# Kernel tuning notes

Hardware: AMD Instinct MI355X
Metric: run time of the kernel (lower is better)

## Reference

```python
import jax, jax.numpy as jnp
import numpy as np

NAN_FRAC = 0.1  # fraction of entries replaced by NaN


def setup_inputs() -> dict:
    key = jax.random.key(0)
    kx, ky, kmx, kmy = jax.random.split(key, 4)
    N, M, D = 4096, 4096, 1024
    X = jax.random.normal(kx, (N, D), dtype=jnp.float32)
    Y = jax.random.normal(ky, (M, D), dtype=jnp.float32)
    X = jnp.where(jax.random.uniform(kmx, (N, D)) < NAN_FRAC, jnp.nan, X)
    Y = jnp.where(jax.random.uniform(kmy, (M, D)) < NAN_FRAC, jnp.nan, Y)
    return {"X": X, "Y": Y}


def reference(X, Y):
    # NaN-masked euclidean distances (sklearn nan_euclidean_distances), squared=False
    missing_X = jnp.isnan(X)                      # [N, D] bool
    missing_Y = jnp.isnan(Y)                      # [M, D] bool
    Xc = jnp.where(missing_X, 0.0, X)
    Yc = jnp.where(missing_Y, 0.0, Y)
    XX = Xc * Xc
    YY = Yc * Yc
    # base squared distances with zero-filled NaNs
    d = (-2.0 * (Xc @ Yc.T)
         + XX.sum(1, keepdims=True)
         + YY.sum(1, keepdims=True).T)            # [N, M]
    # remove contributions where the other side is missing
    d = d - XX @ missing_Y.astype(Xc.dtype).T
    d = d - missing_X.astype(Xc.dtype) @ YY.T
    d = jnp.clip(d, 0.0, None)
    present_X = 1.0 - missing_X.astype(Xc.dtype)  # [N, D]
    present_Y = 1.0 - missing_Y.astype(Xc.dtype)  # [M, D]
    present_count = present_X @ present_Y.T       # [N, M]
    d = jnp.where(present_count == 0, jnp.nan, d)
    pc = jnp.maximum(jnp.asarray(1.0, d.dtype), present_count)
    d = d / pc * X.shape[1]
    return jnp.sqrt(d)
```

## Files before the change

### kernel.cpp

```cpp
#include <hip/hip_runtime.h>
#include <hip/hip_bf16.h>
#include <stdint.h>


typedef __bf16 bf16_t;
typedef __attribute__((ext_vector_type(8))) __bf16 bf16x8;
typedef __attribute__((ext_vector_type(4))) float floatx4;
typedef __attribute__((ext_vector_type(16))) float floatx16;
typedef __attribute__((ext_vector_type(8))) int int32x8;

#define NROWS 4096
#define MCOLS 4096
#define DDIM  1024
#define BM 128
#define BN 128
#define BK 64

#define WS_XX ((uint32_t)0)
#define WS_XC ((uint32_t)(4  << 20))
#define WS_P  ((uint32_t)(8  << 20))
#define WS_YY ((uint32_t)(12 << 20))
#define WS_M2 ((uint32_t)(16 << 20))
#define WS_Q  ((uint32_t)(20 << 20))
#define WS_NEEDED ((size_t)(24 << 20))

#define L_XX 0
#define L_XC 8192
#define L_P  16384
#define L_YY 24576
#define L_M2 32768
#define L_Q  40960

__global__ __launch_bounds__(256)
void convert_planes_mx(const float* __restrict__ X, const float* __restrict__ Y,
                       char* __restrict__ ws) {
    int b = blockIdx.x;
    bool isX = (b < 1024);
    const float* src = isX ? X : Y;
    int rb = isX ? b : b - 1024;
    int row = rb * 4 + (threadIdx.x >> 6);
    int l = threadIdx.x & 63;
    int k0 = l << 4;

    const float4* p = (const float4*)(src + (size_t)row * DDIM + k0);
    float v[16];
    #pragma unroll
    for (int i = 0; i < 4; i++) {
        float4 t = p[i];
        v[4*i+0] = t.x; v[4*i+1] = t.y; v[4*i+2] = t.z; v[4*i+3] = t.w;
    }
    float fa[16], fb[16], fm[16];
    #pragma unroll
    for (int i = 0; i < 16; i++) {
        float x = v[i];
        bool miss = __builtin_isnan(x);
        float c = miss ? 0.f : x;
        fb[i] = c * c;
        fa[i] = isX ? c : (-2.f * c);
        fm[i] = miss ? 0.f : 1.f;
    }
    uint32_t da[4], db[4], dm[4];
    #pragma unroll
    for (int i = 0; i < 4; i++) {
        int r = __builtin_amdgcn_cvt_pk_fp8_f32(fa[4*i], fa[4*i+1], 0, 0);
        r     = __builtin_amdgcn_cvt_pk_fp8_f32(fa[4*i+2], fa[4*i+3], r, 1);
        da[i] = (uint32_t)r;
        int s = __builtin_amdgcn_cvt_pk_fp8_f32(fb[4*i], fb[4*i+1], 0, 0);
        s     = __builtin_amdgcn_cvt_pk_fp8_f32(fb[4*i+2], fb[4*i+3], s, 1);
        db[i] = (uint32_t)s;
        int m = __builtin_amdgcn_cvt_pk_fp8_f32(fm[4*i], fm[4*i+1], 0, 0);
        m     = __builtin_amdgcn_cvt_pk_fp8_f32(fm[4*i+2], fm[4*i+3], m, 1);
        dm[i] = (uint32_t)m;
    }
    uint32_t off8 = (uint32_t)row * 1024u + (uint32_t)(l >> 2) * 64u
                  + (uint32_t)((((l & 3) ^ ((row >> 1) & 3)) << 4));
    uint4 A = make_uint4(da[0], da[1], da[2], da[3]);
    uint4 B = make_uint4(db[0], db[1], db[2], db[3]);
    uint4 M = make_uint4(dm[0], dm[1], dm[2], dm[3]);
    if (isX) {
        *(uint4*)(ws + WS_XC + off8) = A;
        *(uint4*)(ws + WS_XX + off8) = B;
        *(uint4*)(ws + WS_P  + off8) = M;
    } else {
        *(uint4*)(ws + WS_M2 + off8) = A;
        *(uint4*)(ws + WS_YY + off8) = B;
        *(uint4*)(ws + WS_Q  + off8) = M;
    }
}

__device__ __forceinline__ int32x8 ld32B(const char* p0, const char* p1) {
    union { int32x8 v; int4 h[2]; } u;
    u.h[0] = *(const int4*)p0;
    u.h[1] = *(const int4*)p1;
    return u.v;
}

__global__ __launch_bounds__(256, 2)
void nan_euclid_mx(const char* __restrict__ ws, float* __restrict__ out) {
    __shared__ __align__(16) char ldsb[49152];

    const int tid = threadIdx.x, lane = tid & 63, wid = tid >> 6;
    const int l31 = lane & 31, kh = lane >> 5;
    const int wrow = (wid >> 1) * 64, wcol = (wid & 1) * 64;
    const int blockRow = blockIdx.y * BM, blockCol = blockIdx.x * BN;

    uint32_t goff[12];
    #pragma unroll
    for (int t = 0; t < 12; t++) {
        int ch = (wid * 12 + t) * 64 + lane;
        int pl = ch >> 9;
        int c2 = ch & 511;
        int row = c2 >> 2, cc = c2 & 3;
        int rg = (pl < 3 ? blockRow : blockCol) + row;
        uint32_t base = (pl == 0) ? WS_XX : (pl == 1) ? WS_XC : (pl == 2) ? WS_P
                      : (pl == 3) ? WS_YY : (pl == 4) ? WS_M2 : WS_Q;
        goff[t] = base + (uint32_t)rg * 1024u + (uint32_t)(cc << 4);
    }

    int aoff0[2], aoff1[2], boff0[2], boff1[2];
    #pragma unroll
    for (int tt = 0; tt < 2; tt++) {
        int m = wrow + tt * 32 + l31;
        int sw = (m >> 1) & 3;
        aoff0[tt] = m * 64 + (((kh * 2)     ^ sw) << 4);
        aoff1[tt] = m * 64 + (((kh * 2 + 1) ^ sw) << 4);
        int n = wcol + tt * 32 + l31;
        int swn = (n >> 1) & 3;
        boff0[tt] = n * 64 + (((kh * 2)     ^ swn) << 4);
        boff1[tt] = n * 64 + (((kh * 2 + 1) ^ swn) << 4);
    }

    floatx16 acc_d[2][2], acc_c[2][2];
    #pragma unroll
    for (int i = 0; i < 2; i++)
        #pragma unroll
        for (int j = 0; j < 2; j++)
            #pragma unroll
            for (int r = 0; r < 16; r++) { acc_d[i][j][r] = 0.f; acc_c[i][j][r] = 0.f; }

    for (int kc = 0; kc < DDIM / BK; kc++) {
        #pragma unroll
        for (int t = 0; t < 12; t++) {
            __builtin_amdgcn_global_load_lds(
                (const __attribute__((address_space(1))) void*)(ws + goff[t] + kc * 64u),
                (__attribute__((address_space(3))) void*)(ldsb + (uint32_t)((wid * 12 + t) * 1024)),
                16, 0, 0);
        }
        __syncthreads();

        int32x8 axx[2], axc[2], ap[2], byy[2], bm2[2], bq[2];
        #pragma unroll
        for (int tt = 0; tt < 2; tt++) {
            axx[tt] = ld32B(ldsb + L_XX + aoff0[tt], ldsb + L_XX + aoff1[tt]);
            axc[tt] = ld32B(ldsb + L_XC + aoff0[tt], ldsb + L_XC + aoff1[tt]);
            ap [tt] = ld32B(ldsb + L_P  + aoff0[tt], ldsb + L_P  + aoff1[tt]);
            byy[tt] = ld32B(ldsb + L_YY + boff0[tt], ldsb + L_YY + boff1[tt]);
            bm2[tt] = ld32B(ldsb + L_M2 + boff0[tt], ldsb + L_M2 + boff1[tt]);
            bq [tt] = ld32B(ldsb + L_Q  + boff0[tt], ldsb + L_Q  + boff1[tt]);
        }

        #pragma unroll
        for (int tm = 0; tm < 2; tm++)
            #pragma unroll
            for (int tn = 0; tn < 2; tn++)
                acc_d[tm][tn] = __builtin_amdgcn_mfma_scale_f32_32x32x64_f8f6f4(
                    axx[tm], bq[tn], acc_d[tm][tn], 0, 0, 0, 0x7f7f7f7f, 0, 0x7f7f7f7f);
        #pragma unroll
        for (int tm = 0; tm < 2; tm++)
            #pragma unroll
            for (int tn = 0; tn < 2; tn++)
                acc_d[tm][tn] = __builtin_amdgcn_mfma_scale_f32_32x32x64_f8f6f4(
                    ap[tm], byy[tn], acc_d[tm][tn], 0, 0, 0, 0x7f7f7f7f, 0, 0x7f7f7f7f);
        #pragma unroll
        for (int tm = 0; tm < 2; tm++)
            #pragma unroll
            for (int tn = 0; tn < 2; tn++)
                acc_d[tm][tn] = __builtin_amdgcn_mfma_scale_f32_32x32x64_f8f6f4(
                    axc[tm], bm2[tn], acc_d[tm][tn], 0, 0, 0, 0x7f7f7f7f, 0, 0x7f7f7f7f);
        #pragma unroll
        for (int tm = 0; tm < 2; tm++)
            #pragma unroll
            for (int tn = 0; tn < 2; tn++)
                acc_c[tm][tn] = __builtin_amdgcn_mfma_scale_f32_32x32x64_f8f6f4(
                    ap[tm], bq[tn], acc_c[tm][tn], 0, 0, 0, 0x7f7f7f7f, 0, 0x7f7f7f7f);

        __syncthreads();
    }

    #pragma unroll
    for (int tm = 0; tm < 2; tm++) {
        #pragma unroll
        for (int tn = 0; tn < 2; tn++) {
            int col = blockCol + wcol + tn * 32 + l31;
            #pragma unroll
            for (int r = 0; r < 16; r++) {
                int rowl = (r & 3) + 8 * (r >> 2) + 4 * kh;
                int row = blockRow + wrow + tm * 32 + rowl;
                float d = fmaxf(acc_d[tm][tn][r], 0.f);
                float c = acc_c[tm][tn][r];
                float res = (c < 0.5f) ? __builtin_nanf("")
                                       : __builtin_sqrtf(d * (float)DDIM / c);
                out[(size_t)row * MCOLS + col] = res;
            }
        }
    }
}

#define LDK 40
__global__ __launch_bounds__(256, 2)
void nan_euclid_fused(const float* __restrict__ X, const float* __restrict__ Y,
                      float* __restrict__ out) {
    typedef __attribute__((ext_vector_type(4))) __bf16 bf16x4;
    __shared__ bf16_t s_xx[BM * LDK];
    __shared__ bf16_t s_p [BM * LDK];
    __shared__ bf16_t s_xc[BM * LDK];
    __shared__ bf16_t s_q [BN * LDK];
    __shared__ bf16_t s_yy[BN * LDK];
    __shared__ bf16_t s_m2[BN * LDK];

    const int tid  = threadIdx.x;
    const int lane = tid & 63;
    const int wid  = tid >> 6;
    const int quad = lane >> 4;
    const int r16  = lane & 15;
    const int wrow = (wid >> 1) * 64;
    const int wcol = (wid & 1) * 64;
    const int blockRow = blockIdx.y * BM;
    const int blockCol = blockIdx.x * BN;

    floatx4 acc_d[4][4];
    floatx4 acc_c[4][4];
    #pragma unroll
    for (int i = 0; i < 4; i++)
        #pragma unroll
        for (int j = 0; j < 4; j++)
            #pragma unroll
            for (int r = 0; r < 4; r++) { acc_d[i][j][r] = 0.f; acc_c[i][j][r] = 0.f; }

    for (int kc = 0; kc < DDIM / 32; kc++) {
        const int kbase = kc * 32;
        #pragma unroll
        for (int i = 0; i < 4; i++) {
            int idx = tid + 256 * i;
            int row = idx >> 3;
            int c4  = idx & 7;
            const float4 v = *(const float4*)(X + (size_t)(blockRow + row) * DDIM + kbase + c4 * 4);
            bf16x4 vxc, vxx, vp;
            const float xs[4] = {v.x, v.y, v.z, v.w};
            #pragma unroll
            for (int e = 0; e < 4; e++) {
                float x = xs[e];
                bool miss = __builtin_isnan(x);
                float xc = miss ? 0.f : x;
                vxc[e] = (bf16_t)xc;
                vxx[e] = (bf16_t)(xc * xc);
                vp[e]  = miss ? (bf16_t)0.f : (bf16_t)1.f;
            }
            int off = row * LDK + c4 * 4;
            *(bf16x4*)&s_xc[off] = vxc;
            *(bf16x4*)&s_xx[off] = vxx;
            *(bf16x4*)&s_p [off] = vp;
        }
        #pragma unroll
        for (int i = 0; i < 4; i++) {
            int idx = tid + 256 * i;
            int row = idx >> 3;
            int c4  = idx & 7;
            const float4 v = *(const float4*)(Y + (size_t)(blockCol + row) * DDIM + kbase + c4 * 4);
            bf16x4 vq, vyy, vm2;
            const float ys[4] = {v.x, v.y, v.z, v.w};
            #pragma unroll
            for (int e = 0; e < 4; e++) {
                float y = ys[e];
                bool miss = __builtin_isnan(y);
                float yc = miss ? 0.f : y;
                vq[e]  = miss ? (bf16_t)0.f : (bf16_t)1.f;
                vyy[e] = (bf16_t)(yc * yc);
                vm2[e] = (bf16_t)(-2.f * yc);
            }
            int off = row * LDK + c4 * 4;
            *(bf16x4*)&s_q [off] = vq;
            *(bf16x4*)&s_yy[off] = vyy;
            *(bf16x4*)&s_m2[off] = vm2;
        }
        __syncthreads();
        bf16x8 bq[4], byy[4], bm2[4];
        #pragma unroll
        for (int tn = 0; tn < 4; tn++) {
            int off = (wcol + tn * 16 + r16) * LDK + quad * 8;
            bq[tn]  = *(const bf16x8*)&s_q [off];
            byy[tn] = *(const bf16x8*)&s_yy[off];
            bm2[tn] = *(const bf16x8*)&s_m2[off];
        }
        #pragma unroll
        for (int tm = 0; tm < 4; tm++) {
            int off = (wrow + tm * 16 + r16) * LDK + quad * 8;
            bf16x8 axx = *(const bf16x8*)&s_xx[off];
            bf16x8 ap  = *(const bf16x8*)&s_p [off];
            bf16x8 axc = *(const bf16x8*)&s_xc[off];
            #pragma unroll
            for (int tn = 0; tn < 4; tn++) {
                acc_d[tm][tn] = __builtin_amdgcn_mfma_f32_16x16x32_bf16(axx, bq[tn],  acc_d[tm][tn], 0, 0, 0);
                acc_d[tm][tn] = __builtin_amdgcn_mfma_f32_16x16x32_bf16(ap,  byy[tn], acc_d[tm][tn], 0, 0, 0);
                acc_d[tm][tn] = __builtin_amdgcn_mfma_f32_16x16x32_bf16(axc, bm2[tn], acc_d[tm][tn], 0, 0, 0);
                acc_c[tm][tn] = __builtin_amdgcn_mfma_f32_16x16x32_bf16(ap,  bq[tn],  acc_c[tm][tn], 0, 0, 0);
            }
        }
        __syncthreads();
    }
    #pragma unroll
    for (int tm = 0; tm < 4; tm++) {
        #pragma unroll
        for (int tn = 0; tn < 4; tn++) {
            int col = blockCol + wcol + tn * 16 + r16;
            #pragma unroll
            for (int r = 0; r < 4; r++) {
                int row = blockRow + wrow + tm * 16 + quad * 4 + r;
                float d = acc_d[tm][tn][r];
                float c = acc_c[tm][tn][r];
                d = fmaxf(d, 0.f);
                float res = (c < 0.5f) ? __builtin_nanf("")
                                       : __builtin_sqrtf(d * (float)DDIM / c);
                out[(size_t)row * MCOLS + col] = res;
            }
        }
    }
}

extern "C" void kernel_launch(void* const* d_in, const int* in_sizes, int n_in,
                              void* d_out, int out_size, void* d_ws, size_t ws_size,
                              hipStream_t stream) {
    const float* X = (const float*)d_in[0];
    const float* Y = (const float*)d_in[1];
    float* out = (float*)d_out;

    if (ws_size >= WS_NEEDED) {
        char* ws = (char*)d_ws;
        convert_planes_mx<<<dim3(2048), dim3(256), 0, stream>>>(X, Y, ws);
        dim3 grid(MCOLS / BN, NROWS / BM);
        nan_euclid_mx<<<grid, dim3(256), 0, stream>>>(ws, out);
    } else {
        dim3 grid(MCOLS / BN, NROWS / BM);
        nan_euclid_fused<<<grid, dim3(256), 0, stream>>>(X, Y, out);
    }
}
```

Baseline: 164.3 us.

## Double-buffer LDS tiles, swizzle block order, and reshape the fp8 conversion kernel

The main GEMM kernel now keeps two 48KB LDS buffers and issues the global-to-LDS loads for the next K chunk before running the MFMAs on the current one, cutting one barrier per step so memory latency overlaps compute. Blocks are launched on a 1D grid and remapped in strides of eight to improve L2 reuse of the X and Y planes. The conversion kernel now uses one block per row with 4-byte stores instead of 16-byte stores. The 96KB of LDS per block may stop two blocks from sharing a CU as the launch bounds request, and the narrower stores may make the conversion pass slower.

```diff
diff --git a/kernel.cpp b/kernel.cpp
--- a/kernel.cpp
+++ b/kernel.cpp
@@ -30,28 +30,22 @@
 #define L_YY 24576
 #define L_M2 32768
 #define L_Q  40960
+#define BUFSZ 49152
 
 __global__ __launch_bounds__(256)
 void convert_planes_mx(const float* __restrict__ X, const float* __restrict__ Y,
                        char* __restrict__ ws) {
     int b = blockIdx.x;
-    bool isX = (b < 1024);
+    bool isX = (b < 4096);
     const float* src = isX ? X : Y;
-    int rb = isX ? b : b - 1024;
-    int row = rb * 4 + (threadIdx.x >> 6);
-    int l = threadIdx.x & 63;
-    int k0 = l << 4;
-
-    const float4* p = (const float4*)(src + (size_t)row * DDIM + k0);
-    float v[16];
+    int row = isX ? b : b - 4096;
+    int l = threadIdx.x;
+
+    float4 t = *(const float4*)(src + (size_t)row * DDIM + l * 4);
+    float v[4] = {t.x, t.y, t.z, t.w};
+    float fa[4], fb[4], fm[4];
     #pragma unroll
     for (int i = 0; i < 4; i++) {
-        float4 t = p[i];
-        v[4*i+0] = t.x; v[4*i+1] = t.y; v[4*i+2] = t.z; v[4*i+3] = t.w;
-    }
-    float fa[16], fb[16], fm[16];
-    #pragma unroll
-    for (int i = 0; i < 16; i++) {
         float x = v[i];
         bool miss = __builtin_isnan(x);
         float c = miss ? 0.f : x;
@@ -59,32 +53,24 @@
         fa[i] = isX ? c : (-2.f * c);
         fm[i] = miss ? 0.f : 1.f;
     }
-    uint32_t da[4], db[4], dm[4];
-    #pragma unroll
-    for (int i = 0; i < 4; i++) {
-        int r = __builtin_amdgcn_cvt_pk_fp8_f32(fa[4*i], fa[4*i+1], 0, 0);
-        r     = __builtin_amdgcn_cvt_pk_fp8_f32(fa[4*i+2], fa[4*i+3], r, 1);
-        da[i] = (uint32_t)r;
-        int s = __builtin_amdgcn_cvt_pk_fp8_f32(fb[4*i], fb[4*i+1], 0, 0);
-        s     = __builtin_amdgcn_cvt_pk_fp8_f32(fb[4*i+2], fb[4*i+3], s, 1);
-        db[i] = (uint32_t)s;
-        int m = __builtin_amdgcn_cvt_pk_fp8_f32(fm[4*i], fm[4*i+1], 0, 0);
-        m     = __builtin_amdgcn_cvt_pk_fp8_f32(fm[4*i+2], fm[4*i+3], m, 1);
-        dm[i] = (uint32_t)m;
-    }
-    uint32_t off8 = (uint32_t)row * 1024u + (uint32_t)(l >> 2) * 64u
-                  + (uint32_t)((((l & 3) ^ ((row >> 1) & 3)) << 4));
-    uint4 A = make_uint4(da[0], da[1], da[2], da[3]);
-    uint4 B = make_uint4(db[0], db[1], db[2], db[3]);
-    uint4 M = make_uint4(dm[0], dm[1], dm[2], dm[3]);
+    int r = __builtin_amdgcn_cvt_pk_fp8_f32(fa[0], fa[1], 0, 0);
+    r     = __builtin_amdgcn_cvt_pk_fp8_f32(fa[2], fa[3], r, 1);
+    int s = __builtin_amdgcn_cvt_pk_fp8_f32(fb[0], fb[1], 0, 0);
+    s     = __builtin_amdgcn_cvt_pk_fp8_f32(fb[2], fb[3], s, 1);
+    int m = __builtin_amdgcn_cvt_pk_fp8_f32(fm[0], fm[1], 0, 0);
+    m     = __builtin_amdgcn_cvt_pk_fp8_f32(fm[2], fm[3], m, 1);
+
+    uint32_t sw = ((uint32_t)row >> 1) & 3u;
+    uint32_t off = (uint32_t)row * 1024u + (uint32_t)((l >> 4) << 6)
+                 + (((((uint32_t)l >> 2) & 3u) ^ sw) << 4) + (uint32_t)((l & 3) << 2);
     if (isX) {
-        *(uint4*)(ws + WS_XC + off8) = A;
-        *(uint4*)(ws + WS_XX + off8) = B;
-        *(uint4*)(ws + WS_P  + off8) = M;
+        *(uint32_t*)(ws + WS_XC + off) = (uint32_t)r;
+        *(uint32_t*)(ws + WS_XX + off) = (uint32_t)s;
+        *(uint32_t*)(ws + WS_P  + off) = (uint32_t)m;
     } else {
-        *(uint4*)(ws + WS_M2 + off8) = A;
-        *(uint4*)(ws + WS_YY + off8) = B;
-        *(uint4*)(ws + WS_Q  + off8) = M;
+        *(uint32_t*)(ws + WS_M2 + off) = (uint32_t)r;
+        *(uint32_t*)(ws + WS_YY + off) = (uint32_t)s;
+        *(uint32_t*)(ws + WS_Q  + off) = (uint32_t)m;
     }
 }
 
@@ -97,12 +83,16 @@
 
 __global__ __launch_bounds__(256, 2)
 void nan_euclid_mx(const char* __restrict__ ws, float* __restrict__ out) {
-    __shared__ __align__(16) char ldsb[49152];
+    __shared__ __align__(16) char ldsb[2 * BUFSZ];
 
     const int tid = threadIdx.x, lane = tid & 63, wid = tid >> 6;
     const int l31 = lane & 31, kh = lane >> 5;
     const int wrow = (wid >> 1) * 64, wcol = (wid & 1) * 64;
-    const int blockRow = blockIdx.y * BM, blockCol = blockIdx.x * BN;
+
+    const int bid = blockIdx.x;
+    const int swz = (bid & 7) * 128 + (bid >> 3);
+    const int blockRow = (swz >> 5) * BM;
+    const int blockCol = (swz & 31) * BN;
 
     uint32_t goff[12];
     #pragma unroll
@@ -117,17 +107,13 @@
         goff[t] = base + (uint32_t)rg * 1024u + (uint32_t)(cc << 4);
     }
 
-    int aoff0[2], aoff1[2], boff0[2], boff1[2];
+    int aoff[2], boff[2];
     #pragma unroll
     for (int tt = 0; tt < 2; tt++) {
         int m = wrow + tt * 32 + l31;
-        int sw = (m >> 1) & 3;
-        aoff0[tt] = m * 64 + (((kh * 2)     ^ sw) << 4);
-        aoff1[tt] = m * 64 + (((kh * 2 + 1) ^ sw) << 4);
+        aoff[tt] = m * 64 + ((((kh * 2)) ^ ((m >> 1) & 3)) << 4);
         int n = wcol + tt * 32 + l31;
-        int swn = (n >> 1) & 3;
-        boff0[tt] = n * 64 + (((kh * 2)     ^ swn) << 4);
-        boff1[tt] = n * 64 + (((kh * 2 + 1) ^ swn) << 4);
+        boff[tt] = n * 64 + ((((kh * 2)) ^ ((n >> 1) & 3)) << 4);
     }
 
     floatx16 acc_d[2][2], acc_c[2][2];
@@ -138,54 +124,71 @@
             #pragma unroll
             for (int r = 0; r < 16; r++) { acc_d[i][j][r] = 0.f; acc_c[i][j][r] = 0.f; }
 
-    for (int kc = 0; kc < DDIM / BK; kc++) {
-        #pragma unroll
-        for (int t = 0; t < 12; t++) {
-            __builtin_amdgcn_global_load_lds(
-                (const __attribute__((address_space(1))) void*)(ws + goff[t] + kc * 64u),
-                (__attribute__((address_space(3))) void*)(ldsb + (uint32_t)((wid * 12 + t) * 1024)),
-                16, 0, 0);
-        }
-        __syncthreads();
-
-        int32x8 axx[2], axc[2], ap[2], byy[2], bm2[2], bq[2];
-        #pragma unroll
-        for (int tt = 0; tt < 2; tt++) {
-            axx[tt] = ld32B(ldsb + L_XX + aoff0[tt], ldsb + L_XX + aoff1[tt]);
-            axc[tt] = ld32B(ldsb + L_XC + aoff0[tt], ldsb + L_XC + aoff1[tt]);
-            ap [tt] = ld32B(ldsb + L_P  + aoff0[tt], ldsb + L_P  + aoff1[tt]);
-            byy[tt] = ld32B(ldsb + L_YY + boff0[tt], ldsb + L_YY + boff1[tt]);
-            bm2[tt] = ld32B(ldsb + L_M2 + boff0[tt], ldsb + L_M2 + boff1[tt]);
-            bq [tt] = ld32B(ldsb + L_Q  + boff0[tt], ldsb + L_Q  + boff1[tt]);
-        }
-
-        #pragma unroll
-        for (int tm = 0; tm < 2; tm++)
-            #pragma unroll
-            for (int tn = 0; tn < 2; tn++)
-                acc_d[tm][tn] = __builtin_amdgcn_mfma_scale_f32_32x32x64_f8f6f4(
-                    axx[tm], bq[tn], acc_d[tm][tn], 0, 0, 0, 0x7f7f7f7f, 0, 0x7f7f7f7f);
-        #pragma unroll
-        for (int tm = 0; tm < 2; tm++)
-            #pragma unroll
-            for (int tn = 0; tn < 2; tn++)
-                acc_d[tm][tn] = __builtin_amdgcn_mfma_scale_f32_32x32x64_f8f6f4(
-                    ap[tm], byy[tn], acc_d[tm][tn], 0, 0, 0, 0x7f7f7f7f, 0, 0x7f7f7f7f);
-        #pragma unroll
-        for (int tm = 0; tm < 2; tm++)
-            #pragma unroll
-            for (int tn = 0; tn < 2; tn++)
-                acc_d[tm][tn] = __builtin_amdgcn_mfma_scale_f32_32x32x64_f8f6f4(
-                    axc[tm], bm2[tn], acc_d[tm][tn], 0, 0, 0, 0x7f7f7f7f, 0, 0x7f7f7f7f);
-        #pragma unroll
-        for (int tm = 0; tm < 2; tm++)
-            #pragma unroll
-            for (int tn = 0; tn < 2; tn++)
-                acc_c[tm][tn] = __builtin_amdgcn_mfma_scale_f32_32x32x64_f8f6f4(
-                    ap[tm], bq[tn], acc_c[tm][tn], 0, 0, 0, 0x7f7f7f7f, 0, 0x7f7f7f7f);
-
-        __syncthreads();
-    }
+    #pragma unroll
+    for (int t = 0; t < 12; t++) {
+        __builtin_amdgcn_global_load_lds(
+            (const __attribute__((address_space(1))) void*)(ws + goff[t]),
+            (__attribute__((address_space(3))) void*)(ldsb + (uint32_t)((wid * 12 + t) * 1024)),
+            16, 0, 0);
+    }
+    __syncthreads();
+
+#define KSTEP(CURB, NXTB, NKC)                                                     \
+    do {                                                                           \
+        if ((NKC) < DDIM / BK) {                                                   \
+            _Pragma("unroll")                                                      \
+            for (int t = 0; t < 12; t++) {                                         \
+                __builtin_amdgcn_global_load_lds(                                  \
+                    (const __attribute__((address_space(1))) void*)(               \
+                        ws + goff[t] + (uint32_t)(NKC) * 64u),                     \
+                    (__attribute__((address_space(3))) void*)(                     \
+                        ldsb + (NXTB) + (uint32_t)((wid * 12 + t) * 1024)),        \
+                    16, 0, 0);                                                     \
+            }                                                                      \
+        }                                                                          \
+        const char* buf = ldsb + (CURB);                                           \
+        int32x8 axx[2], axc[2], ap[2], byy[2], bm2[2], bq[2];                      \
+        _Pragma("unroll")                                                          \
+        for (int tt = 0; tt < 2; tt++) {                                           \
+            axx[tt] = ld32B(buf + L_XX + aoff[tt], buf + L_XX + (aoff[tt] ^ 16));  \
+            axc[tt] = ld32B(buf + L_XC + aoff[tt], buf + L_XC + (aoff[tt] ^ 16));  \
+            ap [tt] = ld32B(buf + L_P  + aoff[tt], buf + L_P  + (aoff[tt] ^ 16));  \
+            byy[tt] = ld32B(buf + L_YY + boff[tt], buf + L_YY + (boff[tt] ^ 16));  \
+            bm2[tt] = ld32B(buf + L_M2 + boff[tt], buf + L_M2 + (boff[tt] ^ 16));  \
+            bq [tt] = ld32B(buf + L_Q  + boff[tt], buf + L_Q  + (boff[tt] ^ 16));  \
+        }                                                                          \
+        _Pragma("unroll")                                                          \
+        for (int tm = 0; tm < 2; tm++)                                             \
+            _Pragma("unroll")                                                      \
+            for (int tn = 0; tn < 2; tn++)                                         \
+                acc_d[tm][tn] = __builtin_amdgcn_mfma_scale_f32_32x32x64_f8f6f4(   \
+                    axx[tm], bq[tn], acc_d[tm][tn], 0, 0, 0, 0x7f7f7f7f, 0, 0x7f7f7f7f); \
+        _Pragma("unroll")                                                          \
+        for (int tm = 0; tm < 2; tm++)                                             \
+            _Pragma("unroll")                                                      \
+            for (int tn = 0; tn < 2; tn++)                                         \
+                acc_d[tm][tn] = __builtin_amdgcn_mfma_scale_f32_32x32x64_f8f6f4(   \
+                    ap[tm], byy[tn], acc_d[tm][tn], 0, 0, 0, 0x7f7f7f7f, 0, 0x7f7f7f7f); \
+        _Pragma("unroll")                                                          \
+        for (int tm = 0; tm < 2; tm++)                                             \
+            _Pragma("unroll")                                                      \
+            for (int tn = 0; tn < 2; tn++)                                         \
+                acc_d[tm][tn] = __builtin_amdgcn_mfma_scale_f32_32x32x64_f8f6f4(   \
+                    axc[tm], bm2[tn], acc_d[tm][tn], 0, 0, 0, 0x7f7f7f7f, 0, 0x7f7f7f7f); \
+        _Pragma("unroll")                                                          \
+        for (int tm = 0; tm < 2; tm++)                                             \
+            _Pragma("unroll")                                                      \
+            for (int tn = 0; tn < 2; tn++)                                         \
+                acc_c[tm][tn] = __builtin_amdgcn_mfma_scale_f32_32x32x64_f8f6f4(   \
+                    ap[tm], bq[tn], acc_c[tm][tn], 0, 0, 0, 0x7f7f7f7f, 0, 0x7f7f7f7f); \
+        __syncthreads();                                                           \
+    } while (0)
+
+    for (int kc2 = 0; kc2 < DDIM / BK / 2; kc2++) {
+        KSTEP(0,     BUFSZ, 2 * kc2 + 1);
+        KSTEP(BUFSZ, 0,     2 * kc2 + 2);
+    }
+#undef KSTEP
 
     #pragma unroll
     for (int tm = 0; tm < 2; tm++) {
@@ -336,9 +339,8 @@
 
     if (ws_size >= WS_NEEDED) {
         char* ws = (char*)d_ws;
-        convert_planes_mx<<<dim3(2048), dim3(256), 0, stream>>>(X, Y, ws);
-        dim3 grid(MCOLS / BN, NROWS / BM);
-        nan_euclid_mx<<<grid, dim3(256), 0, stream>>>(ws, out);
+        convert_planes_mx<<<dim3(8192), dim3(256), 0, stream>>>(X, Y, ws);
+        nan_euclid_mx<<<dim3(1024), dim3(256), 0, stream>>>(ws, out);
     } else {
         dim3 grid(MCOLS / BN, NROWS / BM);
         nan_euclid_fused<<<grid, dim3(256), 0, stream>>>(X, Y, out);
```

Result: slower. 218.4 us (+32.9%).

## Interleave fp8 planes per row and give each convert block one row

Applied to the files above, without the earlier changes.

The workspace layout changes from six separate plane arrays to a per-row interleaved layout in which each row holds its xx, xc and mask planes contiguously (3 KB per row) for X and Y. The convert kernel now uses one block per row with 4 elements per thread and 4-byte stores, launched over 8192 blocks. The main kernel's global offsets follow the new layout, the LDS second-half offset is computed with an XOR, and MFMA sections are wrapped in s_setprio. The aim is better locality for the per-tile global-to-LDS loads and better balance in the conversion pass, at the cost of smaller 4-byte stores in the convert kernel.

```diff
diff --git a/kernel.cpp b/kernel.cpp
--- a/kernel.cpp
+++ b/kernel.cpp
@@ -16,12 +16,7 @@
 #define BN 128
 #define BK 64
 
-#define WS_XX ((uint32_t)0)
-#define WS_XC ((uint32_t)(4  << 20))
-#define WS_P  ((uint32_t)(8  << 20))
-#define WS_YY ((uint32_t)(12 << 20))
-#define WS_M2 ((uint32_t)(16 << 20))
-#define WS_Q  ((uint32_t)(20 << 20))
+#define WS_YBASE ((uint32_t)(12 << 20))
 #define WS_NEEDED ((size_t)(24 << 20))
 
 #define L_XX 0
@@ -35,23 +30,16 @@
 void convert_planes_mx(const float* __restrict__ X, const float* __restrict__ Y,
                        char* __restrict__ ws) {
     int b = blockIdx.x;
-    bool isX = (b < 1024);
+    bool isX = (b < 4096);
     const float* src = isX ? X : Y;
-    int rb = isX ? b : b - 1024;
-    int row = rb * 4 + (threadIdx.x >> 6);
-    int l = threadIdx.x & 63;
-    int k0 = l << 4;
-
-    const float4* p = (const float4*)(src + (size_t)row * DDIM + k0);
-    float v[16];
+    int row = isX ? b : b - 4096;
+    int l = threadIdx.x;
+
+    float4 t = *(const float4*)(src + (size_t)row * DDIM + l * 4);
+    float v[4] = {t.x, t.y, t.z, t.w};
+    float fa[4], fb[4], fm[4];
     #pragma unroll
     for (int i = 0; i < 4; i++) {
-        float4 t = p[i];
-        v[4*i+0] = t.x; v[4*i+1] = t.y; v[4*i+2] = t.z; v[4*i+3] = t.w;
-    }
-    float fa[16], fb[16], fm[16];
-    #pragma unroll
-    for (int i = 0; i < 16; i++) {
         float x = v[i];
         bool miss = __builtin_isnan(x);
         float c = miss ? 0.f : x;
@@ -59,33 +47,20 @@
         fa[i] = isX ? c : (-2.f * c);
         fm[i] = miss ? 0.f : 1.f;
     }
-    uint32_t da[4], db[4], dm[4];
-    #pragma unroll
-    for (int i = 0; i < 4; i++) {
-        int r = __builtin_amdgcn_cvt_pk_fp8_f32(fa[4*i], fa[4*i+1], 0, 0);
-        r     = __builtin_amdgcn_cvt_pk_fp8_f32(fa[4*i+2], fa[4*i+3], r, 1);
-        da[i] = (uint32_t)r;
-        int s = __builtin_amdgcn_cvt_pk_fp8_f32(fb[4*i], fb[4*i+1], 0, 0);
-        s     = __builtin_amdgcn_cvt_pk_fp8_f32(fb[4*i+2], fb[4*i+3], s, 1);
-        db[i] = (uint32_t)s;
-        int m = __builtin_amdgcn_cvt_pk_fp8_f32(fm[4*i], fm[4*i+1], 0, 0);
-        m     = __builtin_amdgcn_cvt_pk_fp8_f32(fm[4*i+2], fm[4*i+3], m, 1);
-        dm[i] = (uint32_t)m;
-    }
-    uint32_t off8 = (uint32_t)row * 1024u + (uint32_t)(l >> 2) * 64u
-                  + (uint32_t)((((l & 3) ^ ((row >> 1) & 3)) << 4));
-    uint4 A = make_uint4(da[0], da[1], da[2], da[3]);
-    uint4 B = make_uint4(db[0], db[1], db[2], db[3]);
-    uint4 M = make_uint4(dm[0], dm[1], dm[2], dm[3]);
-    if (isX) {
-        *(uint4*)(ws + WS_XC + off8) = A;
-        *(uint4*)(ws + WS_XX + off8) = B;
-        *(uint4*)(ws + WS_P  + off8) = M;
-    } else {
-        *(uint4*)(ws + WS_M2 + off8) = A;
-        *(uint4*)(ws + WS_YY + off8) = B;
-        *(uint4*)(ws + WS_Q  + off8) = M;
-    }
+    int r = __builtin_amdgcn_cvt_pk_fp8_f32(fa[0], fa[1], 0, 0);
+    r     = __builtin_amdgcn_cvt_pk_fp8_f32(fa[2], fa[3], r, 1);
+    int s = __builtin_amdgcn_cvt_pk_fp8_f32(fb[0], fb[1], 0, 0);
+    s     = __builtin_amdgcn_cvt_pk_fp8_f32(fb[2], fb[3], s, 1);
+    int m = __builtin_amdgcn_cvt_pk_fp8_f32(fm[0], fm[1], 0, 0);
+    m     = __builtin_amdgcn_cvt_pk_fp8_f32(fm[2], fm[3], m, 1);
+
+    uint32_t sw = ((uint32_t)row >> 1) & 3u;
+    uint32_t off = (uint32_t)((l >> 4) << 6)
+                 + (((((uint32_t)l >> 2) & 3u) ^ sw) << 4) + (uint32_t)((l & 3) << 2);
+    uint32_t base = (isX ? 0u : WS_YBASE) + (uint32_t)row * 3072u;
+    *(uint32_t*)(ws + base +    0u + off) = (uint32_t)s;
+    *(uint32_t*)(ws + base + 1024u + off) = (uint32_t)r;
+    *(uint32_t*)(ws + base + 2048u + off) = (uint32_t)m;
 }
 
 __device__ __forceinline__ int32x8 ld32B(const char* p0, const char* p1) {
@@ -111,23 +86,20 @@
         int pl = ch >> 9;
         int c2 = ch & 511;
         int row = c2 >> 2, cc = c2 & 3;
-        int rg = (pl < 3 ? blockRow : blockCol) + row;
-        uint32_t base = (pl == 0) ? WS_XX : (pl == 1) ? WS_XC : (pl == 2) ? WS_P
-                      : (pl == 3) ? WS_YY : (pl == 4) ? WS_M2 : WS_Q;
-        goff[t] = base + (uint32_t)rg * 1024u + (uint32_t)(cc << 4);
-    }
-
-    int aoff0[2], aoff1[2], boff0[2], boff1[2];
+        bool isA = (pl < 3);
+        int rg = (isA ? blockRow : blockCol) + row;
+        int pl_loc = isA ? pl : pl - 3;
+        goff[t] = (isA ? 0u : WS_YBASE) + (uint32_t)rg * 3072u
+                + (uint32_t)pl_loc * 1024u + (uint32_t)(cc << 4);
+    }
+
+    int aoff[2], boff[2];
     #pragma unroll
     for (int tt = 0; tt < 2; tt++) {
         int m = wrow + tt * 32 + l31;
-        int sw = (m >> 1) & 3;
-        aoff0[tt] = m * 64 + (((kh * 2)     ^ sw) << 4);
-        aoff1[tt] = m * 64 + (((kh * 2 + 1) ^ sw) << 4);
+        aoff[tt] = m * 64 + ((((kh * 2)) ^ ((m >> 1) & 3)) << 4);
         int n = wcol + tt * 32 + l31;
-        int swn = (n >> 1) & 3;
-        boff0[tt] = n * 64 + (((kh * 2)     ^ swn) << 4);
-        boff1[tt] = n * 64 + (((kh * 2 + 1) ^ swn) << 4);
+        boff[tt] = n * 64 + ((((kh * 2)) ^ ((n >> 1) & 3)) << 4);
     }
 
     floatx16 acc_d[2][2], acc_c[2][2];
@@ -142,7 +114,7 @@
         #pragma unroll
         for (int t = 0; t < 12; t++) {
             __builtin_amdgcn_global_load_lds(
-                (const __attribute__((address_space(1))) void*)(ws + goff[t] + kc * 64u),
+                (const __attribute__((address_space(1))) void*)(ws + goff[t] + (uint32_t)kc * 64u),
                 (__attribute__((address_space(3))) void*)(ldsb + (uint32_t)((wid * 12 + t) * 1024)),
                 16, 0, 0);
         }
@@ -151,14 +123,15 @@
         int32x8 axx[2], axc[2], ap[2], byy[2], bm2[2], bq[2];
         #pragma unroll
         for (int tt = 0; tt < 2; tt++) {
-            axx[tt] = ld32B(ldsb + L_XX + aoff0[tt], ldsb + L_XX + aoff1[tt]);
-            axc[tt] = ld32B(ldsb + L_XC + aoff0[tt], ldsb + L_XC + aoff1[tt]);
-            ap [tt] = ld32B(ldsb + L_P  + aoff0[tt], ldsb + L_P  + aoff1[tt]);
-            byy[tt] = ld32B(ldsb + L_YY + boff0[tt], ldsb + L_YY + boff1[tt]);
-            bm2[tt] = ld32B(ldsb + L_M2 + boff0[tt], ldsb + L_M2 + boff1[tt]);
-            bq [tt] = ld32B(ldsb + L_Q  + boff0[tt], ldsb + L_Q  + boff1[tt]);
-        }
-
+            axx[tt] = ld32B(ldsb + L_XX + aoff[tt], ldsb + L_XX + (aoff[tt] ^ 16));
+            axc[tt] = ld32B(ldsb + L_XC + aoff[tt], ldsb + L_XC + (aoff[tt] ^ 16));
+            ap [tt] = ld32B(ldsb + L_P  + aoff[tt], ldsb + L_P  + (aoff[tt] ^ 16));
+            byy[tt] = ld32B(ldsb + L_YY + boff[tt], ldsb + L_YY + (boff[tt] ^ 16));
+            bm2[tt] = ld32B(ldsb + L_M2 + boff[tt], ldsb + L_M2 + (boff[tt] ^ 16));
+            bq [tt] = ld32B(ldsb + L_Q  + boff[tt], ldsb + L_Q  + (boff[tt] ^ 16));
+        }
+
+        __builtin_amdgcn_s_setprio(1);
         #pragma unroll
         for (int tm = 0; tm < 2; tm++)
             #pragma unroll
@@ -183,6 +156,7 @@
             for (int tn = 0; tn < 2; tn++)
                 acc_c[tm][tn] = __builtin_amdgcn_mfma_scale_f32_32x32x64_f8f6f4(
                     ap[tm], bq[tn], acc_c[tm][tn], 0, 0, 0, 0x7f7f7f7f, 0, 0x7f7f7f7f);
+        __builtin_amdgcn_s_setprio(0);
 
         __syncthreads();
     }
@@ -336,7 +310,7 @@
 
     if (ws_size >= WS_NEEDED) {
         char* ws = (char*)d_ws;
-        convert_planes_mx<<<dim3(2048), dim3(256), 0, stream>>>(X, Y, ws);
+        convert_planes_mx<<<dim3(8192), dim3(256), 0, stream>>>(X, Y, ws);
         dim3 grid(MCOLS / BN, NROWS / BM);
         nan_euclid_mx<<<grid, dim3(256), 0, stream>>>(ws, out);
     } else {
```

Result: slower. 198.8 us (+21.0%).
